# Optimization experiments

Measured on AMD Instinct MI355X. Metric: run time of the kernel, lower is better.

Reference implementation:

```python
import jax, jax.numpy as jnp
import numpy as np

H = 8
DK = 32
D_MODEL = H * DK


def _leaky(x):
    # LeakyReLU(negative_slope=0.1)
    return jnp.where(x > 0, x, 0.1 * x)


def _edge_feat(p_edge, W1, b1, W2, b2):
    # p_edge: [b, d_edge, n, n] -> [b, h, d_k, n, n]
    e = jnp.transpose(p_edge, (0, 2, 3, 1))          # [b, n, n, d_edge]
    e = _leaky(e @ W1 + b1) @ W2 + b2                # [b, n, n, d_model]
    b, n = e.shape[0], e.shape[1]
    e = e.reshape(b, n, n, H, DK)
    return jnp.transpose(e, (0, 3, 4, 1, 2))          # [b, h, d_k, n, n]


def setup_inputs() -> dict:
    key = jax.random.key(0)
    ks = jax.random.split(key, 24)
    b, n, d_model, d_edge, d_hidden = 2, 512, 256, 40, 32
    s = 0.05
    return {
        "query": jax.random.normal(ks[0], (b, n, d_model), jnp.float32),
        "key_": jax.random.normal(ks[1], (b, n, d_model), jnp.float32),
        "value": jax.random.normal(ks[2], (b, n, d_model), jnp.float32),
        "edges_att": jax.random.normal(ks[3], (b, d_edge, n, n), jnp.float32),
        "mask": jax.random.randint(ks[4], (b, n), 0, 2, jnp.int32),
        "Wq": jax.random.normal(ks[5], (d_model, d_model), jnp.float32) * s,
        "bq": jax.random.normal(ks[6], (d_model,), jnp.float32) * s,
        "Wk": jax.random.normal(ks[7], (d_model, d_model), jnp.float32) * s,
        "bk": jax.random.normal(ks[8], (d_model,), jnp.float32) * s,
        "Wv": jax.random.normal(ks[9], (d_model, d_model), jnp.float32) * s,
        "bv": jax.random.normal(ks[10], (d_model,), jnp.float32) * s,
        "Wo": jax.random.normal(ks[11], (d_model, d_model), jnp.float32) * s,
        "bo": jax.random.normal(ks[12], (d_model,), jnp.float32) * s,
        "rkW1": jax.random.normal(ks[13], (d_edge, d_hidden), jnp.float32) * s,
        "rkb1": jax.random.normal(ks[14], (d_hidden,), jnp.float32) * s,
        "rkW2": jax.random.normal(ks[15], (d_hidden, d_model), jnp.float32) * s,
        "rkb2": jax.random.normal(ks[16], (d_model,), jnp.float32) * s,
        "rvW1": jax.random.normal(ks[17], (d_edge, d_hidden), jnp.float32) * s,
        "rvb1": jax.random.normal(ks[18], (d_hidden,), jnp.float32) * s,
        "rvW2": jax.random.normal(ks[19], (d_hidden, d_model), jnp.float32) * s,
        "rvb2": jax.random.normal(ks[20], (d_model,), jnp.float32) * s,
        "u": jax.random.normal(ks[21], (H, DK), jnp.float32) * s,
        "v": jax.random.normal(ks[22], (H, DK), jnp.float32) * s,
    }


def reference(query, key_, value, edges_att, mask,
              Wq, bq, Wk, bk, Wv, bv, Wo, bo,
              rkW1, rkb1, rkW2, rkb2, rvW1, rvb1, rvW2, rvb2, u, v):
    b, n, _ = query.shape

    def proj(x, W, bb):
        return jnp.transpose((x @ W + bb).reshape(b, n, H, DK), (0, 2, 1, 3))  # [b,h,n,d_k]

    q = proj(query, Wq, bq)
    k = proj(key_, Wk, bk)
    val = proj(value, Wv, bv)

    relK = _edge_feat(edges_att, rkW1, rkb1, rkW2, rkb2)  # [b,h,d_k,n,n]
    relV = _edge_feat(edges_att, rvW1, rvb1, rvW2, rvb2)  # [b,h,d_k,n,n]

    inv = 1.0 / jnp.sqrt(jnp.asarray(DK, q.dtype))
    s1 = jnp.einsum('bhid,bhjd->bhij', q, k) * inv
    s2 = jnp.einsum('bhid,bhdij->bhij', q + k, relK) * inv
    s3 = jnp.einsum('bhid,hd->bhi', k, u)[..., None]      # broadcast over j
    s4 = jnp.einsum('bhdij,hd->bhij', relK, v)
    scores = s1 + s2 + s3 + s4
    scores = jnp.where(mask[:, None, None, :] == 0, jnp.asarray(-1e12, scores.dtype), scores)
    p = jax.nn.softmax(scores, axis=-1)                    # [b,h,n,n]

    o = jnp.einsum('bhij,bhjd->bhid', p, val) + jnp.einsum('bhij,bhdij->bhid', p, relV)
    x = jnp.transpose(o, (0, 2, 1, 3)).reshape(b, n, D_MODEL)
    return x @ Wo + bo
```

## Files before the change

kernel.cpp:

```cpp
#include <hip/hip_runtime.h>
#include <hip/hip_bf16.h>

#define HH 8
#define DKK 32
#define DM 256
#define NN 512
#define DE 40
#define DHID 32
#define CH 128

typedef __attribute__((ext_vector_type(4))) short short4v;
typedef __attribute__((ext_vector_type(8))) short short8v;
typedef __attribute__((ext_vector_type(4))) float f32x4;

__device__ __forceinline__ unsigned short f2bf(float x) {
    union { __hip_bfloat16 h; unsigned short u; } c;
    c.h = __float2bfloat16(x);
    return c.u;
}
__device__ __forceinline__ float bf2f(unsigned short u) {
    return __uint_as_float(((unsigned int)u) << 16);
}
__device__ __forceinline__ float bf_lo(unsigned int u){ return __uint_as_float(u << 16); }
__device__ __forceinline__ float bf_hi(unsigned int u){ return __uint_as_float(u & 0xffff0000u); }
__device__ __forceinline__ unsigned int pack2bf(float a, float b) {
    return (unsigned int)f2bf(a) | ((unsigned int)f2bf(b) << 16);
}
__device__ __forceinline__ short8v ld8(const unsigned short* p) {
    short4v lo = *(const short4v*)p;
    short4v hi = *(const short4v*)(p + 4);
    short8v r;
    r[0]=lo[0]; r[1]=lo[1]; r[2]=lo[2]; r[3]=lo[3];
    r[4]=hi[0]; r[5]=hi[1]; r[6]=hi[2]; r[7]=hi[3];
    return r;
}

__global__ __launch_bounds__(256) void proj_kernel(
    const float* __restrict__ query, const float* __restrict__ key_,
    const float* __restrict__ value,
    const float* __restrict__ Wq, const float* __restrict__ bq,
    const float* __restrict__ Wk, const float* __restrict__ bk,
    const float* __restrict__ Wv, const float* __restrict__ bv,
    float* __restrict__ Q, float* __restrict__ K, float* __restrict__ V,
    int grpPerMat)
{
    const int m  = blockIdx.x / grpPerMat;
    const int r0 = (blockIdx.x % grpPerMat) * 4;
    const float* x; const float* W; const float* bb; float* dst;
    if (m == 0)      { x = query; W = Wq; bb = bq; dst = Q; }
    else if (m == 1) { x = key_;  W = Wk; bb = bk; dst = K; }
    else             { x = value; W = Wv; bb = bv; dst = V; }
    const int c = threadIdx.x;
    const float b0 = bb[c];
    float a0 = b0, a1 = b0, a2 = b0, a3 = b0;
    for (int k = 0; k < DM; ++k) {
        const float w = W[k*DM + c];
        a0 = fmaf(x[(size_t)(r0+0)*DM + k], w, a0);
        a1 = fmaf(x[(size_t)(r0+1)*DM + k], w, a1);
        a2 = fmaf(x[(size_t)(r0+2)*DM + k], w, a2);
        a3 = fmaf(x[(size_t)(r0+3)*DM + k], w, a3);
    }
    dst[(size_t)(r0+0)*DM + c] = a0;
    dst[(size_t)(r0+1)*DM + c] = a1;
    dst[(size_t)(r0+2)*DM + c] = a2;
    dst[(size_t)(r0+3)*DM + c] = a3;
}

__global__ __launch_bounds__(256) void pre_kernel(
    const float* __restrict__ Q, const float* __restrict__ K,
    const float* __restrict__ vvec,
    const float* __restrict__ rkW2, const float* __restrict__ rkb2,
    const float* __restrict__ rkW1, const float* __restrict__ rvW1,
    const float* __restrict__ rkb1, const float* __restrict__ rvb1,
    unsigned short* __restrict__ s1, float* __restrict__ gkw,
    unsigned short* __restrict__ w1w, float* __restrict__ biasw)
{
    const int bid = blockIdx.x;
    const int tid = threadIdx.x;
    __shared__ __align__(16) float sh[2*64*33];

    if (bid < 1024) {
        float (*Qt)[33] = (float(*)[33])sh;
        float (*Kt)[33] = (float(*)[33])(sh + 64*33);
        const int bh = bid >> 6, b = bh >> 3, hh = bh & 7;
        const int bx = bid & 63;
        const int ti = (bx >> 3) * 64, tj = (bx & 7) * 64;
        const int c = tid & 31, r0 = tid >> 5;
#pragma unroll
        for (int s = 0; s < 8; ++s) {
            Qt[r0 + 8*s][c] = Q[(size_t)(b*NN + ti + r0 + 8*s)*DM + hh*DKK + c];
            Kt[r0 + 8*s][c] = K[(size_t)(b*NN + tj + r0 + 8*s)*DM + hh*DKK + c];
        }
        __syncthreads();
        const int tx = tid & 15, ty = tid >> 4;
        float acc[4][4] = {};
#pragma unroll
        for (int k = 0; k < DKK; ++k) {
            float qv[4], kv[4];
#pragma unroll
            for (int u = 0; u < 4; ++u) { qv[u] = Qt[ty*4+u][k]; kv[u] = Kt[tx*4+u][k]; }
#pragma unroll
            for (int ri = 0; ri < 4; ++ri)
#pragma unroll
                for (int cj = 0; cj < 4; ++cj)
                    acc[ri][cj] = fmaf(qv[ri], kv[cj], acc[ri][cj]);
        }
        const float inv = 0.17677669529663687f;
#pragma unroll
        for (int ri = 0; ri < 4; ++ri) {
            ushort4 o;
            o.x = f2bf(acc[ri][0]*inv); o.y = f2bf(acc[ri][1]*inv);
            o.z = f2bf(acc[ri][2]*inv); o.w = f2bf(acc[ri][3]*inv);
            *(ushort4*)(s1 + ((size_t)(b*HH + hh)*NN + ti + ty*4 + ri)*NN + tj + tx*4) = o;
        }
    } else if (bid < 2048) {
        const int bi = bid - 1024;
        const int h = tid >> 5, l32 = tid & 31;
        const float inv = 0.17677669529663687f;
        float* wf = sh;
        wf[tid] = inv*(Q[(size_t)bi*DM + tid] + K[(size_t)bi*DM + tid]) + vvec[tid];
        __syncthreads();
        float acc = 0.f;
#pragma unroll
        for (int d4 = 0; d4 < DKK/4; ++d4) {
            const float4 w4 = *(const float4*)(rkW2 + (size_t)l32*DM + h*DKK + d4*4);
            const float4 f4 = *(const float4*)(&wf[h*DKK + d4*4]);
            acc = fmaf(w4.x, f4.x, acc); acc = fmaf(w4.y, f4.y, acc);
            acc = fmaf(w4.z, f4.z, acc); acc = fmaf(w4.w, f4.w, acc);
        }
        gkw[(size_t)bi*264 + tid] = acc;
        if (tid < HH) {
            float a2 = 0.f;
#pragma unroll
            for (int d = 0; d < DKK; ++d)
                a2 = fmaf(rkb2[tid*DKK + d], wf[tid*DKK + d], a2);
            gkw[(size_t)bi*264 + 256 + tid] = a2;
        }
    } else {
        const int n = tid >> 2, qd = tid & 3;
#pragma unroll
        for (int kk = 0; kk < 17; ++kk) {
            const int k = qd*17 + kk;
            float v = 0.f;
            if (k < DE) v = (n < 32) ? rkW1[k*DHID + n] : rvW1[k*DHID + (n-32)];
            w1w[n*68 + k] = f2bf(v);
        }
        if (tid < 64) biasw[tid] = (tid < 32) ? rkb1[tid] : rvb1[tid-32];
    }
}

__global__ __launch_bounds__(256, 5) void chunk_kernel(
    const float* __restrict__ edges, const int* __restrict__ mask,
    const float* __restrict__ V,
    const unsigned short* __restrict__ s1u,
    const unsigned short* __restrict__ w1w, const float* __restrict__ biasw,
    const float* __restrict__ gkw,
    float* __restrict__ ws_m, float* __restrict__ ws_z,
    float* __restrict__ ws_A4, float* __restrict__ ws_O4)
{
    const int bid = blockIdx.x;
    const int bi = bid >> 2, cq = bid & 3;
    const int b  = bi >> 9;
    const int i  = bi & 511;
    const int j0 = cq*CH;
    const int tid = threadIdx.x;
    const int h = tid >> 5, l32 = tid & 31;
    const int wid = tid >> 6, lane = tid & 63;
    const int g = lane >> 4, q16 = lane & 15;
    const int team = tid >> 6, qq = tid & 63, hq = qq >> 3;
    const int jj = tid & 127, half = tid >> 7;

    __shared__ __align__(16) unsigned char uni[17408];
    __shared__ __align__(16) unsigned short W1bf[64*68];
    __shared__ __align__(16) float sc[HH*132];
    __shared__ __align__(16) float gKs[HH*DKK];
    __shared__ float c0Ks[HH];
    __shared__ float bias_l[64];

    unsigned short* E   = (unsigned short*)uni;
    unsigned short* hvT = (unsigned short*)uni;
    unsigned short* hk  = (unsigned short*)(uni + 8448);
    unsigned short* pb  = (unsigned short*)(uni + 8448);

    const size_t ebase = (size_t)b*DE*NN*NN + (size_t)i*NN;

    float ev[20];
    {
        const float* ep = edges + ebase + j0 + jj;
#pragma unroll
        for (int u = 0; u < 20; ++u) ev[u] = ep[(size_t)(half*20+u)*NN*NN];
    }
    unsigned short s1v[4];
    {
        const unsigned short* s1b = s1u + (size_t)b*HH*NN*NN + (size_t)i*NN + j0 + jj;
#pragma unroll
        for (int u = 0; u < 4; ++u) s1v[u] = s1b[(size_t)(half*4+u)*NN*NN];
    }
    const int mk = mask[b*NN + j0 + jj];

    {
        const unsigned int* src = (const unsigned int*)w1w;
        unsigned int* dst = (unsigned int*)W1bf;
#pragma unroll
        for (int u = tid; u < 2176; u += 256) dst[u] = src[u];
        const float* gsrc = gkw + (size_t)bi*264;
        gKs[tid] = gsrc[tid];
        if (tid < HH) c0Ks[tid] = gsrc[256 + tid];
        if (tid < 64) bias_l[tid] = biasw[tid];

        unsigned int* Ed = (unsigned int*)&E[jj*68 + half*20];
#pragma unroll
        for (int u = 0; u < 10; ++u) Ed[u] = pack2bf(ev[2*u], ev[2*u+1]);
        if (half) {
            unsigned int* Ez = (unsigned int*)&E[jj*68 + 40];
#pragma unroll
            for (int z = 0; z < 12; ++z) Ez[z] = 0u;
        }
    }
    __syncthreads();

    float biasv[4];
#pragma unroll
    for (int nt = 0; nt < 4; ++nt) biasv[nt] = bias_l[nt*16 + q16];

    f32x4 acc[2][4];
#pragma unroll
    for (int jt = 0; jt < 2; ++jt) {
        const int jn = wid*32 + jt*16 + q16;
        short8v a0 = ld8(&E[jn*68 + g*8]);
        short8v a1 = ld8(&E[jn*68 + 32 + g*8]);
#pragma unroll
        for (int nt = 0; nt < 4; ++nt) {
            const unsigned short* wp = &W1bf[(q16 + nt*16)*68 + g*8];
            f32x4 c;
            c[0] = biasv[nt]; c[1] = biasv[nt]; c[2] = biasv[nt]; c[3] = biasv[nt];
            c = __builtin_amdgcn_mfma_f32_16x16x32_bf16(a0, ld8(wp), c, 0, 0, 0);
            c = __builtin_amdgcn_mfma_f32_16x16x32_bf16(a1, ld8(wp + 32), c, 0, 0, 0);
            acc[jt][nt] = c;
        }
    }
    __syncthreads();

#pragma unroll
    for (int jt = 0; jt < 2; ++jt) {
        const int jw = wid*32 + jt*16 + g*4;
#pragma unroll
        for (int nt = 0; nt < 4; ++nt) {
#pragma unroll
            for (int r = 0; r < 4; ++r) {
                float x = acc[jt][nt][r];
                x = x > 0.f ? x : 0.1f*x;
                const unsigned short us = f2bf(x);
                const int n = nt*16 + q16;
                if (n < 32) hk[(jw+r)*34 + n] = us;
                else        hvT[(n-32)*132 + (jw+r)] = us;
            }
        }
    }
    __syncthreads();

    {
        unsigned int hku[16];
#pragma unroll
        for (int d = 0; d < 16; ++d) hku[d] = *(const unsigned int*)&hk[jj*34 + 2*d];
        float racc[4];
#pragma unroll
        for (int u = 0; u < 4; ++u) racc[u] = c0Ks[half*4 + u];
#pragma unroll
        for (int d = 0; d < 16; ++d) {
            const float lo = bf_lo(hku[d]), hi = bf_hi(hku[d]);
#pragma unroll
            for (int u = 0; u < 4; ++u) {
                const int hh = half*4 + u;
                racc[u] = fmaf(gKs[hh*DKK + 2*d],     lo, racc[u]);
                racc[u] = fmaf(gKs[hh*DKK + 2*d + 1], hi, racc[u]);
            }
        }
#pragma unroll
        for (int u = 0; u < 4; ++u) {
            const int hh = half*4 + u;
            float r = racc[u] + bf2f(s1v[u]);
            if (mk == 0) r = -1e12f;
            sc[hh*132 + jj] = r;
        }
    }
    __syncthreads();

    {
        float sv[4];
        float mc = -3e38f;
#pragma unroll
        for (int k = 0; k < 4; ++k) { sv[k] = sc[h*132 + l32 + 32*k]; mc = fmaxf(mc, sv[k]); }
#pragma unroll
        for (int off = 16; off; off >>= 1) mc = fmaxf(mc, __shfl_xor(mc, off, 32));
        float zc = 0.f;
#pragma unroll
        for (int k = 0; k < 4; ++k) {
            const float e = __expf(sv[k] - mc);
            pb[h*132 + l32 + 32*k] = f2bf(e);
            zc += e;
        }
#pragma unroll
        for (int off = 16; off; off >>= 1) zc += __shfl_xor(zc, off, 32);
        if (l32 == 0) {
            ws_m[(size_t)bid*8 + h] = mc;
            ws_z[(size_t)bid*8 + h] = zc;
        }
    }
    __syncthreads();

    f32x4 ca0 = {0.f,0.f,0.f,0.f}, ca1 = {0.f,0.f,0.f,0.f};
    {
        short8v pA = ld8(&pb[q16*132 + wid*32 + g*8]);
        short8v b0 = ld8(&hvT[q16*132 + wid*32 + g*8]);
        short8v b1 = ld8(&hvT[(16+q16)*132 + wid*32 + g*8]);
        ca0 = __builtin_amdgcn_mfma_f32_16x16x32_bf16(pA, b0, ca0, 0, 0, 0);
        ca1 = __builtin_amdgcn_mfma_f32_16x16x32_bf16(pA, b1, ca1, 0, 0, 0);
    }
    float aO0 = 0.f, aO1 = 0.f, aO2 = 0.f, aO3 = 0.f;
    {
        const float* vrow = V + (size_t)b*NN*DM + (size_t)(j0 + team)*DM + qq*4;
        const unsigned short* ph = pb + hq*132 + team;
#pragma unroll 4
        for (int it = 0; it < 32; ++it) {
            const float p = bf2f(ph[4*it]);
            const float4 v4 = *(const float4*)(vrow + (size_t)it*4*DM);
            aO0 = fmaf(p, v4.x, aO0); aO1 = fmaf(p, v4.y, aO1);
            aO2 = fmaf(p, v4.z, aO2); aO3 = fmaf(p, v4.w, aO3);
        }
    }

    if (g < 2) {
        float* pa = ws_A4 + ((size_t)bid*4 + wid)*256;
#pragma unroll
        for (int r = 0; r < 4; ++r) {
            const int hrow = g*4 + r;
            pa[hrow*32 + q16]      = ca0[r];
            pa[hrow*32 + 16 + q16] = ca1[r];
        }
    }
    *(float4*)(ws_O4 + ((size_t)bid*4 + team)*256 + qq*4) = make_float4(aO0, aO1, aO2, aO3);
}

__global__ __launch_bounds__(256) void combine_kernel(
    const float* __restrict__ rvW2, const float* __restrict__ rvb2,
    const float* __restrict__ Wo, const float* __restrict__ bo,
    const float* __restrict__ ws_m, const float* __restrict__ ws_z,
    const float* __restrict__ ws_A4, const float* __restrict__ ws_O4,
    float* __restrict__ out)
{
    const int bi0 = blockIdx.x * 2;
    const int tid = threadIdx.x;
    const int h = tid >> 5;
    __shared__ float A_l[2][DM], o_l[2][DM];
    __shared__ float wqs[2][4][HH], rzs[2][HH];

    if (tid < 16) {
        const int r = tid >> 3, hh = tid & 7;
        const int bi = bi0 + r;
        float mv[4], zv[4];
#pragma unroll
        for (int q = 0; q < 4; ++q) {
            mv[q] = ws_m[(size_t)(bi*4+q)*8 + hh];
            zv[q] = ws_z[(size_t)(bi*4+q)*8 + hh];
        }
        const float mm = fmaxf(fmaxf(mv[0], mv[1]), fmaxf(mv[2], mv[3]));
        float zt = 0.f;
#pragma unroll
        for (int q = 0; q < 4; ++q) {
            const float w = __expf(mv[q] - mm);
            wqs[r][q][hh] = w;
            zt = fmaf(zv[q], w, zt);
        }
        rzs[r][hh] = 1.f / zt;
    }
    __syncthreads();

    float o1v[2];
#pragma unroll
    for (int r = 0; r < 2; ++r) {
        const int bi = bi0 + r;
        const float rz = rzs[r][h];
        float A = 0.f, o1 = 0.f;
#pragma unroll
        for (int q = 0; q < 4; ++q) {
            const float w = wqs[r][q][h];
            const float* pa = ws_A4 + ((size_t)(bi*4+q))*1024 + tid;
            const float* po = ws_O4 + ((size_t)(bi*4+q))*1024 + tid;
            A  = fmaf(w, (pa[0]+pa[256]) + (pa[512]+pa[768]), A);
            o1 = fmaf(w, (po[0]+po[256]) + (po[512]+po[768]), o1);
        }
        A_l[r][tid] = A * rz;
        o1v[r] = o1 * rz;
    }
    __syncthreads();

#pragma unroll
    for (int r = 0; r < 2; ++r) {
        float o2 = rvb2[tid];
#pragma unroll
        for (int t = 0; t < DHID; ++t)
            o2 = fmaf(A_l[r][h*DKK + t], rvW2[(size_t)t*DM + tid], o2);
        o_l[r][tid] = o1v[r] + o2;
    }
    __syncthreads();

    float acc0 = bo[tid], acc1 = acc0;
#pragma unroll 4
    for (int k = 0; k < DM; ++k) {
        const float w = Wo[(size_t)k*DM + tid];
        acc0 = fmaf(o_l[0][k], w, acc0);
        acc1 = fmaf(o_l[1][k], w, acc1);
    }
    out[(size_t)(bi0+0)*DM + tid] = acc0;
    out[(size_t)(bi0+1)*DM + tid] = acc1;
}

extern "C" void kernel_launch(void* const* d_in, const int* in_sizes, int n_in,
                              void* d_out, int out_size, void* d_ws, size_t ws_size,
                              hipStream_t stream) {
    const float* query = (const float*)d_in[0];
    const float* key_  = (const float*)d_in[1];
    const float* value = (const float*)d_in[2];
    const float* edges = (const float*)d_in[3];
    const int*   mask  = (const int*)d_in[4];
    const float* Wq = (const float*)d_in[5];
    const float* bq = (const float*)d_in[6];
    const float* Wk = (const float*)d_in[7];
    const float* bk = (const float*)d_in[8];
    const float* Wv = (const float*)d_in[9];
    const float* bv = (const float*)d_in[10];
    const float* Wo = (const float*)d_in[11];
    const float* bo = (const float*)d_in[12];
    const float* rkW1 = (const float*)d_in[13];
    const float* rkb1 = (const float*)d_in[14];
    const float* rkW2 = (const float*)d_in[15];
    const float* rkb2 = (const float*)d_in[16];
    const float* rvW1 = (const float*)d_in[17];
    const float* rvb1 = (const float*)d_in[18];
    const float* rvW2 = (const float*)d_in[19];
    const float* rvb2 = (const float*)d_in[20];
    const float* vvec = (const float*)d_in[22];

    const int rows = in_sizes[0] / DM;
    const int nchunk = rows * 4;

    float* Qw    = (float*)d_ws;
    float* Kw    = Qw + (size_t)rows*DM;
    float* Vw    = Kw + (size_t)rows*DM;
    float* gkw   = Vw + (size_t)rows*DM;
    float* biasw = gkw + (size_t)rows*264;
    float* ws_m  = biasw + 64;
    float* ws_z  = ws_m + (size_t)nchunk*8;
    float* ws_A4 = ws_z + (size_t)nchunk*8;
    float* ws_O4 = ws_A4 + (size_t)nchunk*1024;
    unsigned short* s1u = (unsigned short*)(ws_O4 + (size_t)nchunk*1024);
    unsigned short* w1w = s1u + (size_t)2*HH*NN*NN;

    hipLaunchKernelGGL(proj_kernel, dim3(3*rows/4), dim3(256), 0, stream,
                       query, key_, value, Wq, bq, Wk, bk, Wv, bv,
                       Qw, Kw, Vw, rows/4);
    hipLaunchKernelGGL(pre_kernel, dim3(2*rows + 1), dim3(256), 0, stream,
                       Qw, Kw, vvec, rkW2, rkb2, rkW1, rvW1, rkb1, rvb1,
                       s1u, gkw, w1w, biasw);
    hipLaunchKernelGGL(chunk_kernel, dim3(nchunk), dim3(256), 0, stream,
                       edges, mask, Vw, s1u, w1w, biasw, gkw,
                       ws_m, ws_z, ws_A4, ws_O4);
    hipLaunchKernelGGL(combine_kernel, dim3(rows/2), dim3(256), 0, stream,
                       rvW2, rvb2, Wo, bo, ws_m, ws_z, ws_A4, ws_O4, (float*)d_out);
}
```

Baseline: 112.8 us.

## Drop W1 LDS staging, reduce per-wave partials in LDS before global write

The chunk kernel no longer copies the bf16 W1 weights and bias into shared memory. The MFMA operands and bias are read directly from global memory, where they should stay in cache. The four per-wave A and O partial sums are now reduced in shared memory before writing, so each block writes a quarter of the previous workspace. The combine kernel reads correspondingly less. Occupancy hint rises from 5 to 6 blocks per CU, helped by the smaller LDS footprint, at the cost of two extra barriers and uncoalesced global loads for the weight operands.

```diff
diff --git a/kernel.cpp b/kernel.cpp
--- a/kernel.cpp
+++ b/kernel.cpp
@@ -149,14 +149,14 @@
     }
 }
 
-__global__ __launch_bounds__(256, 5) void chunk_kernel(
+__global__ __launch_bounds__(256, 6) void chunk_kernel(
     const float* __restrict__ edges, const int* __restrict__ mask,
     const float* __restrict__ V,
     const unsigned short* __restrict__ s1u,
     const unsigned short* __restrict__ w1w, const float* __restrict__ biasw,
     const float* __restrict__ gkw,
     float* __restrict__ ws_m, float* __restrict__ ws_z,
-    float* __restrict__ ws_A4, float* __restrict__ ws_O4)
+    float* __restrict__ ws_A, float* __restrict__ ws_O)
 {
     const int bid = blockIdx.x;
     const int bi = bid >> 2, cq = bid & 3;
@@ -171,16 +171,16 @@
     const int jj = tid & 127, half = tid >> 7;
 
     __shared__ __align__(16) unsigned char uni[17408];
-    __shared__ __align__(16) unsigned short W1bf[64*68];
     __shared__ __align__(16) float sc[HH*132];
     __shared__ __align__(16) float gKs[HH*DKK];
     __shared__ float c0Ks[HH];
-    __shared__ float bias_l[64];
 
     unsigned short* E   = (unsigned short*)uni;
     unsigned short* hvT = (unsigned short*)uni;
     unsigned short* hk  = (unsigned short*)(uni + 8448);
     unsigned short* pb  = (unsigned short*)(uni + 8448);
+    float* paccA = (float*)uni;
+    float* po    = (float*)(uni + 4096);
 
     const size_t ebase = (size_t)b*DE*NN*NN + (size_t)i*NN;
 
@@ -197,16 +197,14 @@
         for (int u = 0; u < 4; ++u) s1v[u] = s1b[(size_t)(half*4+u)*NN*NN];
     }
     const int mk = mask[b*NN + j0 + jj];
-
-    {
-        const unsigned int* src = (const unsigned int*)w1w;
-        unsigned int* dst = (unsigned int*)W1bf;
-#pragma unroll
-        for (int u = tid; u < 2176; u += 256) dst[u] = src[u];
+    float biasv[4];
+#pragma unroll
+    for (int nt = 0; nt < 4; ++nt) biasv[nt] = biasw[nt*16 + q16];
+
+    {
         const float* gsrc = gkw + (size_t)bi*264;
         gKs[tid] = gsrc[tid];
         if (tid < HH) c0Ks[tid] = gsrc[256 + tid];
-        if (tid < 64) bias_l[tid] = biasw[tid];
 
         unsigned int* Ed = (unsigned int*)&E[jj*68 + half*20];
 #pragma unroll
@@ -218,10 +216,6 @@
         }
     }
     __syncthreads();
-
-    float biasv[4];
-#pragma unroll
-    for (int nt = 0; nt < 4; ++nt) biasv[nt] = bias_l[nt*16 + q16];
 
     f32x4 acc[2][4];
 #pragma unroll
@@ -231,7 +225,7 @@
         short8v a1 = ld8(&E[jn*68 + 32 + g*8]);
 #pragma unroll
         for (int nt = 0; nt < 4; ++nt) {
-            const unsigned short* wp = &W1bf[(q16 + nt*16)*68 + g*8];
+            const unsigned short* wp = w1w + (q16 + nt*16)*68 + g*8;
             f32x4 c;
             c[0] = biasv[nt]; c[1] = biasv[nt]; c[2] = biasv[nt]; c[3] = biasv[nt];
             c = __builtin_amdgcn_mfma_f32_16x16x32_bf16(a0, ld8(wp), c, 0, 0, 0);
@@ -329,24 +323,28 @@
             aO2 = fmaf(p, v4.z, aO2); aO3 = fmaf(p, v4.w, aO3);
         }
     }
+    __syncthreads();
 
     if (g < 2) {
-        float* pa = ws_A4 + ((size_t)bid*4 + wid)*256;
 #pragma unroll
         for (int r = 0; r < 4; ++r) {
             const int hrow = g*4 + r;
-            pa[hrow*32 + q16]      = ca0[r];
-            pa[hrow*32 + 16 + q16] = ca1[r];
-        }
-    }
-    *(float4*)(ws_O4 + ((size_t)bid*4 + team)*256 + qq*4) = make_float4(aO0, aO1, aO2, aO3);
+            paccA[wid*256 + hrow*32 + q16]      = ca0[r];
+            paccA[wid*256 + hrow*32 + 16 + q16] = ca1[r];
+        }
+    }
+    *(float4*)(po + team*256 + qq*4) = make_float4(aO0, aO1, aO2, aO3);
+    __syncthreads();
+
+    ws_A[(size_t)bid*256 + tid] = paccA[tid] + paccA[256+tid] + paccA[512+tid] + paccA[768+tid];
+    ws_O[(size_t)bid*256 + tid] = po[tid] + po[256+tid] + po[512+tid] + po[768+tid];
 }
 
 __global__ __launch_bounds__(256) void combine_kernel(
     const float* __restrict__ rvW2, const float* __restrict__ rvb2,
     const float* __restrict__ Wo, const float* __restrict__ bo,
     const float* __restrict__ ws_m, const float* __restrict__ ws_z,
-    const float* __restrict__ ws_A4, const float* __restrict__ ws_O4,
+    const float* __restrict__ ws_A, const float* __restrict__ ws_O,
     float* __restrict__ out)
 {
     const int bi0 = blockIdx.x * 2;
@@ -385,10 +383,8 @@
 #pragma unroll
         for (int q = 0; q < 4; ++q) {
             const float w = wqs[r][q][h];
-            const float* pa = ws_A4 + ((size_t)(bi*4+q))*1024 + tid;
-            const float* po = ws_O4 + ((size_t)(bi*4+q))*1024 + tid;
-            A  = fmaf(w, (pa[0]+pa[256]) + (pa[512]+pa[768]), A);
-            o1 = fmaf(w, (po[0]+po[256]) + (po[512]+po[768]), o1);
+            A  = fmaf(w, ws_A[(size_t)(bi*4+q)*256 + tid], A);
+            o1 = fmaf(w, ws_O[(size_t)(bi*4+q)*256 + tid], o1);
         }
         A_l[r][tid] = A * rz;
         o1v[r] = o1 * rz;
@@ -452,9 +448,9 @@
     float* biasw = gkw + (size_t)rows*264;
     float* ws_m  = biasw + 64;
     float* ws_z  = ws_m + (size_t)nchunk*8;
-    float* ws_A4 = ws_z + (size_t)nchunk*8;
-    float* ws_O4 = ws_A4 + (size_t)nchunk*1024;
-    unsigned short* s1u = (unsigned short*)(ws_O4 + (size_t)nchunk*1024);
+    float* ws_A  = ws_z + (size_t)nchunk*8;
+    float* ws_O  = ws_A + (size_t)nchunk*256;
+    unsigned short* s1u = (unsigned short*)(ws_O + (size_t)nchunk*256);
     unsigned short* w1w = s1u + (size_t)2*HH*NN*NN;
 
     hipLaunchKernelGGL(proj_kernel, dim3(3*rows/4), dim3(256), 0, stream,
@@ -465,7 +461,7 @@
                        s1u, gkw, w1w, biasw);
     hipLaunchKernelGGL(chunk_kernel, dim3(nchunk), dim3(256), 0, stream,
                        edges, mask, Vw, s1u, w1w, biasw, gkw,
-                       ws_m, ws_z, ws_A4, ws_O4);
+                       ws_m, ws_z, ws_A, ws_O);
     hipLaunchKernelGGL(combine_kernel, dim3(rows/2), dim3(256), 0, stream,
-                       rvW2, rvb2, Wo, bo, ws_m, ws_z, ws_A4, ws_O4, (float*)d_out);
-}
+                       rvW2, rvb2, Wo, bo, ws_m, ws_z, ws_A, ws_O, (float*)d_out);
+}
```

Result: faster. 96.85 us (median of 2 runs) (-14.2%).
